# Kernel optimization log

Hardware: AMD Instinct MI355X
Metric: run time of the kernel (lower is better)

Reference implementation:

```python
import jax, jax.numpy as jnp
import numpy as np

D = 1024
KERNEL = 4

def setup_inputs() -> dict:
    key = jax.random.key(0)
    ks = jax.random.split(key, 8)
    B, L, d = 4, 8192, D
    x = jax.random.normal(ks[0], (B, L, d), dtype=jnp.float32)
    conv_weight = jax.random.normal(ks[1], (d, 1, KERNEL), dtype=jnp.float32) * 0.02
    conv_bias = jnp.zeros((d,), dtype=jnp.float32)
    lim = 1.0 / np.sqrt(d)
    Wr_w = jax.random.uniform(ks[2], (d, d), jnp.float32, -lim, lim)
    Wr_b = jax.random.uniform(ks[3], (d,), jnp.float32, -lim, lim)
    Wi_w = jax.random.uniform(ks[4], (d, d), jnp.float32, -lim, lim)
    Wi_b = jax.random.uniform(ks[5], (d,), jnp.float32, -lim, lim)
    log_a = jnp.full((d,), 7.5, dtype=jnp.float32)
    out_w = jax.random.uniform(ks[6], (d, d), jnp.float32, -lim, lim)
    norm_w = jnp.ones((d,), dtype=jnp.float32)
    return {"x": x, "conv_weight": conv_weight, "conv_bias": conv_bias,
            "Wr_w": Wr_w, "Wr_b": Wr_b, "Wi_w": Wi_w, "Wi_b": Wi_b,
            "log_a": log_a, "out_w": out_w, "norm_w": norm_w}

def _causal_depthwise_conv(x, w, b):
    # x: [B,L,d], w: [d,1,K], b: [d]. out[t] = sum_k w[:,0,k] * x[t-3+k] + b
    B, L, d = x.shape
    xp = jnp.pad(x, ((0, 0), (KERNEL - 1, 0), (0, 0)))
    out = b[None, None, :]
    for k in range(KERNEL):  # small fixed kernel loop
        out = out + xp[:, k:k + L, :] * w[:, 0, k][None, None, :]
    return out

def _parallel_scan(a_t, b_t):
    # h_t = a_t * h_{t-1} + b_t via log-space cumsum; float32 throughout
    a = a_t.astype(jnp.float32)
    b = b_t.astype(jnp.float32)
    log_A = jnp.clip(jnp.cumsum(jnp.log(jnp.clip(a, 1e-7)), axis=1), -80.0, None)
    A = jnp.exp(log_A)
    h = A * jnp.cumsum(b * jnp.exp(-log_A), axis=1)
    return h.astype(a_t.dtype)

def _rmsnorm(x, w, eps=1e-6):
    ms = jnp.mean(jnp.square(x.astype(jnp.float32)), axis=-1, keepdims=True)
    return (x * jax.lax.rsqrt(ms + eps)).astype(x.dtype) * w

def reference(x, conv_weight, conv_bias, Wr_w, Wr_b, Wi_w, Wi_b, log_a, out_w, norm_w):
    x_conv = _causal_depthwise_conv(x, conv_weight, conv_bias)          # [B,L,d]
    r_t = jax.nn.sigmoid(x_conv @ Wr_w.T + Wr_b)
    i_t = jax.nn.sigmoid(x_conv @ Wi_w.T + Wi_b)
    a_base = jax.nn.sigmoid(log_a.astype(jnp.float32)).astype(x.dtype)
    a_t = jnp.power(a_base[None, None, :], 8.0 * r_t)
    b_t = jnp.sqrt(jnp.clip(1.0 - a_t * a_t, 1e-6, None)) * (i_t * x_conv)
    h = _parallel_scan(a_t, b_t)
    return _rmsnorm(h @ out_w.T, norm_w)
```

## Files before the change

### kernel.cpp

```cpp
#include <hip/hip_runtime.h>
#include <hip/hip_bf16.h>

#define D 1024
#define KW 4
#define SEQL 8192
#define BATCH 4
#define MROWS (BATCH*SEQL)
#define SEG 32
#define NSEG (SEQL/SEG)
#define NCHAIN (BATCH*D)

using bf16 = __hip_bfloat16;
typedef __attribute__((ext_vector_type(8))) short bf16x8_t;
typedef __attribute__((ext_vector_type(4))) float f32x4_t;

__device__ __forceinline__ float sigmoid_f(float x){ return 1.0f/(1.0f + __expf(-x)); }

__device__ __forceinline__ void gload_lds16(const bf16* g, bf16* l){
  __builtin_amdgcn_global_load_lds(
    (const __attribute__((address_space(1))) unsigned int*)g,
    (__attribute__((address_space(3))) unsigned int*)l,
    16, 0, 0);
}

__device__ __forceinline__ void bf16x2_unpack(unsigned int u, float& lo, float& hi){
  union { unsigned int i; float f; } a, b;
  a.i = (u & 0xffffu) << 16;
  b.i = u & 0xffff0000u;
  lo = a.f; hi = b.f;
}
__device__ __forceinline__ unsigned int bf16x2_pack(float lo, float hi){
  unsigned short l = __builtin_bit_cast(unsigned short, __float2bfloat16(lo));
  unsigned short h = __builtin_bit_cast(unsigned short, __float2bfloat16(hi));
  return (unsigned int)l | ((unsigned int)h << 16);
}

__global__ __launch_bounds__(256) void prep_k(const float* __restrict__ Wr, const float* __restrict__ Wi,
                                              const float* __restrict__ Wrb, const float* __restrict__ Wib,
                                              const float* __restrict__ Wo,
                                              bf16* __restrict__ W1, bf16* __restrict__ Wob,
                                              float* __restrict__ b1){
  int idx = blockIdx.x*256 + threadIdx.x;
  if (idx < 2*D*D){
    int n = idx >> 10;
    float v = (n < D) ? Wr[idx] : Wi[idx - D*D];
    W1[idx] = __float2bfloat16(v);
  } else if (idx < 3*D*D){
    int j = idx - 2*D*D;
    Wob[j] = __float2bfloat16(Wo[j]);
  }
  if (idx < 2*D){
    b1[idx] = (idx < D) ? Wrb[idx] : Wib[idx - D];
  }
}

__global__ __launch_bounds__(256) void conv_k(const float* __restrict__ x, const float* __restrict__ w,
                                              const float* __restrict__ bias,
                                              unsigned int* __restrict__ xcb){
  int idx = blockIdx.x*256 + threadIdx.x;
  int c4 = idx & 255;
  int c  = c4 * 4;
  int mm = idx >> 8;
  int m  = mm * 2;
  int l  = m & (SEQL-1);
  const float* wp = w + c*KW;
  f32x4_t t0 = *(const f32x4_t*)(wp);
  f32x4_t t1 = *(const f32x4_t*)(wp + 4);
  f32x4_t t2 = *(const f32x4_t*)(wp + 8);
  f32x4_t t3 = *(const f32x4_t*)(wp + 12);
  f32x4_t bb = *(const f32x4_t*)(bias + c);
  const float* xm = x + (size_t)m*D + c;
  f32x4_t z  = (f32x4_t){0.f,0.f,0.f,0.f};
  f32x4_t r4 = *(const f32x4_t*)(xm + D);
  f32x4_t r3 = *(const f32x4_t*)(xm);
  f32x4_t r2 = (l>=1)? *(const f32x4_t*)(xm - D)   : z;
  f32x4_t r1 = (l>=2)? *(const f32x4_t*)(xm - 2*D) : z;
  f32x4_t r0 = (l>=3)? *(const f32x4_t*)(xm - 3*D) : z;
  float a0 = bb[0] + t0[0]*r0[0] + t0[1]*r1[0] + t0[2]*r2[0] + t0[3]*r3[0];
  float a1 = bb[1] + t1[0]*r0[1] + t1[1]*r1[1] + t1[2]*r2[1] + t1[3]*r3[1];
  float a2 = bb[2] + t2[0]*r0[2] + t2[1]*r1[2] + t2[2]*r2[2] + t2[3]*r3[2];
  float a3 = bb[3] + t3[0]*r0[3] + t3[1]*r1[3] + t3[2]*r2[3] + t3[3]*r3[3];
  float b0 = bb[0] + t0[0]*r1[0] + t0[1]*r2[0] + t0[2]*r3[0] + t0[3]*r4[0];
  float b1v= bb[1] + t1[0]*r1[1] + t1[1]*r2[1] + t1[2]*r3[1] + t1[3]*r4[1];
  float b2 = bb[2] + t2[0]*r1[2] + t2[1]*r2[2] + t2[2]*r3[2] + t2[3]*r4[2];
  float b3 = bb[3] + t3[0]*r1[3] + t3[1]*r2[3] + t3[2]*r3[3] + t3[3]*r4[3];
  uint2 o0, o1;
  o0.x = bf16x2_pack(a0, a1); o0.y = bf16x2_pack(a2, a3);
  o1.x = bf16x2_pack(b0, b1v); o1.y = bf16x2_pack(b2, b3);
  *(uint2*)(xcb + (size_t)m*512 + 2*c4)       = o0;
  *(uint2*)(xcb + (size_t)(m+1)*512 + 2*c4)   = o1;
}

template<typename OutT> __device__ __forceinline__ void store_cvt(OutT* p, float v);
template<> __device__ __forceinline__ void store_cvt<float>(float* p, float v){ *p = v; }
template<> __device__ __forceinline__ void store_cvt<bf16>(bf16* p, float v){ *p = __float2bfloat16(v); }

#define MFMA_BF16(a,b,c) __builtin_amdgcn_mfma_f32_16x16x32_bf16((a),(b),(c),0,0,0)

#define GPHASE(buf, q, STAGE_STMT, WAIT_STMT) do{                         \
    bf16x8_t a0 = rdA(buf, 2*(q),   0);                                   \
    bf16x8_t a1 = rdA(buf, 2*(q),   1);                                   \
    bf16x8_t a2 = rdA(buf, 2*(q)+1, 0);                                   \
    bf16x8_t a3 = rdA(buf, 2*(q)+1, 1);                                   \
    if ((q) == 0){                                                        \
      b00 = rdB(buf,0,0); b01 = rdB(buf,0,1);                             \
      b10 = rdB(buf,1,0); b11 = rdB(buf,1,1);                             \
      b20 = rdB(buf,2,0); b21 = rdB(buf,2,1);                             \
      b30 = rdB(buf,3,0); b31 = rdB(buf,3,1);                             \
    }                                                                     \
    STAGE_STMT;                                                           \
    WAIT_STMT;                                                            \
    __builtin_amdgcn_s_barrier();                                         \
    asm volatile("s_waitcnt lgkmcnt(0)" ::: "memory");                    \
    __builtin_amdgcn_s_setprio(1);                                        \
    acc[2*(q)  ][0] = MFMA_BF16(a0, b00, acc[2*(q)  ][0]);                \
    acc[2*(q)  ][1] = MFMA_BF16(a0, b10, acc[2*(q)  ][1]);                \
    acc[2*(q)  ][2] = MFMA_BF16(a0, b20, acc[2*(q)  ][2]);                \
    acc[2*(q)  ][3] = MFMA_BF16(a0, b30, acc[2*(q)  ][3]);                \
    acc[2*(q)+1][0] = MFMA_BF16(a2, b00, acc[2*(q)+1][0]);                \
    acc[2*(q)+1][1] = MFMA_BF16(a2, b10, acc[2*(q)+1][1]);                \
    acc[2*(q)+1][2] = MFMA_BF16(a2, b20, acc[2*(q)+1][2]);                \
    acc[2*(q)+1][3] = MFMA_BF16(a2, b30, acc[2*(q)+1][3]);                \
    acc[2*(q)  ][0] = MFMA_BF16(a1, b01, acc[2*(q)  ][0]);                \
    acc[2*(q)  ][1] = MFMA_BF16(a1, b11, acc[2*(q)  ][1]);                \
    acc[2*(q)  ][2] = MFMA_BF16(a1, b21, acc[2*(q)  ][2]);                \
    acc[2*(q)  ][3] = MFMA_BF16(a1, b31, acc[2*(q)  ][3]);                \
    acc[2*(q)+1][0] = MFMA_BF16(a3, b01, acc[2*(q)+1][0]);                \
    acc[2*(q)+1][1] = MFMA_BF16(a3, b11, acc[2*(q)+1][1]);                \
    acc[2*(q)+1][2] = MFMA_BF16(a3, b21, acc[2*(q)+1][2]);                \
    acc[2*(q)+1][3] = MFMA_BF16(a3, b31, acc[2*(q)+1][3]);                \
    __builtin_amdgcn_s_setprio(0);                                        \
    __builtin_amdgcn_s_barrier();                                         \
}while(0)

#define WAIT_STEADY do{ if (it + 1 < nIter) asm volatile("s_waitcnt vmcnt(4)" ::: "memory"); \
                        else                asm volatile("s_waitcnt vmcnt(0)" ::: "memory"); }while(0)

template<typename OutT, bool HB>
__global__ __launch_bounds__(512, 2) void gemm256(const bf16* __restrict__ A, const bf16* __restrict__ B,
                                                  const float* __restrict__ bias, OutT* __restrict__ C,
                                                  int M, int N, int K){
  __shared__ alignas(128) bf16 Asm[2][256*64];
  __shared__ alignas(128) bf16 Bsm[2][256*64];
  const int t    = threadIdx.x;
  const int wave = t >> 6, lane = t & 63;
  const int wm   = wave >> 2, wn = wave & 3;
  const int lrow = lane & 15, quad = lane >> 4;

  const int nbn = N >> 8;
  const int cpx = gridDim.x >> 3;
  const int bid = blockIdx.x;
  const int swz = (bid & 7) * cpx + (bid >> 3);
  const int m0  = (swz / nbn) << 8;
  const int n0  = (swz % nbn) << 8;

  const int srow = wave*8 + (lane >> 3);
  const int scol = (((lane & 7) ^ (srow & 7)) << 3);

  auto stageA = [&](int tile, int half, int buf){
    const bf16* g = A + (size_t)(m0 + half*128 + srow)*K + tile*64 + scol;
    bf16* l = &Asm[buf][half*128*64 + wave*8*64];
    gload_lds16(g, l);
    gload_lds16(g + (size_t)64*K, l + 64*64);
  };
  auto stageB = [&](int tile, int half, int buf){
    const bf16* g = B + (size_t)(n0 + half*128 + srow)*K + tile*64 + scol;
    bf16* l = &Bsm[buf][half*128*64 + wave*8*64];
    gload_lds16(g, l);
    gload_lds16(g + (size_t)64*K, l + 64*64);
  };
  auto rdA = [&](int buf, int fi, int ks)->bf16x8_t{
    return *(const bf16x8_t*)&Asm[buf][(wm*128 + fi*16 + lrow)*64 + ((((ks)*4 + quad) ^ (lrow & 7)) << 3)];
  };
  auto rdB = [&](int buf, int j, int ks)->bf16x8_t{
    return *(const bf16x8_t*)&Bsm[buf][(wn*64 + j*16 + lrow)*64 + ((((ks)*4 + quad) ^ (lrow & 7)) << 3)];
  };

  f32x4_t acc[8][4];
  #pragma unroll
  for (int i=0;i<8;i++)
    #pragma unroll
    for (int j=0;j<4;j++) acc[i][j] = (f32x4_t){0.f,0.f,0.f,0.f};
  bf16x8_t b00,b01,b10,b11,b20,b21,b30,b31;

  const int nt    = K >> 6;
  const int nIter = nt >> 1;

  stageB(0, 0, 0); stageB(0, 1, 0);
  stageA(0, 0, 0); stageA(0, 1, 0);
  stageB(1, 0, 1); stageB(1, 1, 1);
  asm volatile("s_waitcnt vmcnt(4)" ::: "memory");
  __builtin_amdgcn_s_barrier();

  for (int it = 0; it < nIter; ++it){
    const int t1 = 2*it + 1, t2 = 2*it + 2, t3 = 2*it + 3;
    const bool ok2 = (t2 < nt), ok3 = (t3 < nt);
    GPHASE(0, 0, stageA(t1, 0, 1), );
    GPHASE(0, 1, stageA(t1, 1, 1), );
    GPHASE(0, 2, if (ok2) stageB(t2, 0, 0), );
    GPHASE(0, 3, if (ok2) stageB(t2, 1, 0), WAIT_STEADY);
    GPHASE(1, 0, if (ok2) stageA(t2, 0, 0), );
    GPHASE(1, 1, if (ok2) stageA(t2, 1, 0), );
    GPHASE(1, 2, if (ok3) stageB(t3, 0, 1), );
    GPHASE(1, 3, if (ok3) stageB(t3, 1, 1), WAIT_STEADY);
  }

  constexpr int ROWP = 256 + 16/(int)sizeof(OutT);
  OutT* tile = (OutT*)&Asm[0][0];
  const int trow = t >> 4;
  const int tcol = (t & 15) * 16;
  float bvj[4];
  #pragma unroll
  for (int j=0;j<4;j++) bvj[j] = HB ? bias[n0 + wn*64 + j*16 + lrow] : 0.f;
  const int grow = m0 + (trow >> 4)*128 + (trow & 15);

  #pragma unroll
  for (int i=0;i<8;i++){
    __builtin_amdgcn_s_barrier();
    #pragma unroll
    for (int j=0;j<4;j++){
      int lcol = wn*64 + j*16 + lrow;
      #pragma unroll
      for (int r=0;r<4;r++)
        store_cvt(&tile[(wm*16 + quad*4 + r)*ROWP + lcol], acc[i][j][r] + bvj[j]);
    }
    __builtin_amdgcn_s_barrier();
    const int4* lp = (const int4*)&tile[trow*ROWP + tcol];
    int4* gp = (int4*)&C[(size_t)(grow + i*16)*N + n0 + tcol];
    #pragma unroll
    for (int q=0; q<(int)sizeof(OutT); ++q) gp[q] = lp[q];
  }
}

__global__ __launch_bounds__(256) void scan1_k(const unsigned int* __restrict__ ri,
                                               const unsigned int* __restrict__ xcb,
                                               const float* __restrict__ log_a,
                                               float* __restrict__ AprodT, float* __restrict__ HendT){
  int idx = blockIdx.x*256 + threadIdx.x;
  int c4 = idx & 255;
  int c  = c4*4;
  int bs = idx >> 8;
  int s  = bs & (NSEG-1);
  int b  = bs >> 8;
  size_t m0 = (size_t)b*SEQL + (size_t)s*SEG;
  f32x4_t la = *(const f32x4_t*)(log_a + c);
  float c1[4];
  #pragma unroll
  for (int j=0;j<4;j++) c1[j] = -8.f * log1pf(__expf(-la[j]));
  float A[4] = {1.f,1.f,1.f,1.f};
  float h[4] = {0.f,0.f,0.f,0.f};
  #pragma unroll 4
  for (int l=0; l<SEG; l++){
    size_t m = m0 + l;
    uint2 uzr = *(const uint2*)(ri  + m*1024 + 2*c4);
    uint2 uzi = *(const uint2*)(ri  + m*1024 + 512 + 2*c4);
    uint2 uxv = *(const uint2*)(xcb + m*512  + 2*c4);
    float zr[4], zi[4], xv[4];
    bf16x2_unpack(uzr.x, zr[0], zr[1]); bf16x2_unpack(uzr.y, zr[2], zr[3]);
    bf16x2_unpack(uzi.x, zi[0], zi[1]); bf16x2_unpack(uzi.y, zi[2], zi[3]);
    bf16x2_unpack(uxv.x, xv[0], xv[1]); bf16x2_unpack(uxv.y, xv[2], xv[3]);
    #pragma unroll
    for (int j=0;j<4;j++){
      float a  = __expf(c1[j] * sigmoid_f(zr[j]));
      float bt = sqrtf(fmaxf(1.f - a*a, 1e-6f)) * sigmoid_f(zi[j]) * xv[j];
      A[j] *= a;
      h[j]  = fmaf(a, h[j], bt);
    }
  }
  size_t tbase = (size_t)s*NCHAIN + (size_t)b*D + c;
  *(f32x4_t*)(AprodT + tbase) = (f32x4_t){A[0],A[1],A[2],A[3]};
  *(f32x4_t*)(HendT  + tbase) = (f32x4_t){h[0],h[1],h[2],h[3]};
}

__global__ __launch_bounds__(256) void scan2_k(const float* __restrict__ AprodT, const float* __restrict__ HendT,
                                               float* __restrict__ carryT){
  int gid   = blockIdx.x*256 + threadIdx.x;
  int chain = gid >> 6;
  int lane  = gid & 63;
  int s0    = lane*4;
  float a[4], e[4];
  #pragma unroll
  for (int k=0;k<4;k++){
    a[k] = AprodT[(size_t)(s0+k)*NCHAIN + chain];
    e[k] = HendT [(size_t)(s0+k)*NCHAIN + chain];
  }
  float A = a[0], H = e[0];
  #pragma unroll
  for (int k=1;k<4;k++){ H = fmaf(a[k], H, e[k]); A *= a[k]; }
  #pragma unroll
  for (int off=1; off<64; off<<=1){
    float Ao = __shfl_up(A, off, 64);
    float Ho = __shfl_up(H, off, 64);
    if (lane >= off){ H = fmaf(A, Ho, H); A = A*Ao; }
  }
  float Hx = __shfl_up(H, 1, 64);
  if (lane == 0) Hx = 0.f;
  float h = Hx;
  #pragma unroll
  for (int k=0;k<4;k++){
    carryT[(size_t)(s0+k)*NCHAIN + chain] = h;
    h = fmaf(a[k], h, e[k]);
  }
}

__global__ __launch_bounds__(256) void scan3_k(const unsigned int* __restrict__ ri,
                                               unsigned int* xcb,
                                               const float* __restrict__ log_a, const float* __restrict__ carryT){
  int idx = blockIdx.x*256 + threadIdx.x;
  int c4 = idx & 255;
  int c  = c4*4;
  int bs = idx >> 8;
  int s  = bs & (NSEG-1);
  int b  = bs >> 8;
  size_t m0 = (size_t)b*SEQL + (size_t)s*SEG;
  f32x4_t la = *(const f32x4_t*)(log_a + c);
  float c1[4];
  #pragma unroll
  for (int j=0;j<4;j++) c1[j] = -8.f * log1pf(__expf(-la[j]));
  f32x4_t h4 = *(const f32x4_t*)(carryT + (size_t)s*NCHAIN + (size_t)b*D + c);
  float h[4] = {h4[0], h4[1], h4[2], h4[3]};
  #pragma unroll 4
  for (int l=0; l<SEG; l++){
    size_t m = m0 + l;
    uint2 uzr = *(const uint2*)(ri  + m*1024 + 2*c4);
    uint2 uzi = *(const uint2*)(ri  + m*1024 + 512 + 2*c4);
    uint2 uxv = *(const uint2*)(xcb + m*512  + 2*c4);
    float zr[4], zi[4], xv[4];
    bf16x2_unpack(uzr.x, zr[0], zr[1]); bf16x2_unpack(uzr.y, zr[2], zr[3]);
    bf16x2_unpack(uzi.x, zi[0], zi[1]); bf16x2_unpack(uzi.y, zi[2], zi[3]);
    bf16x2_unpack(uxv.x, xv[0], xv[1]); bf16x2_unpack(uxv.y, xv[2], xv[3]);
    #pragma unroll
    for (int j=0;j<4;j++){
      float a  = __expf(c1[j] * sigmoid_f(zr[j]));
      float bt = sqrtf(fmaxf(1.f - a*a, 1e-6f)) * sigmoid_f(zi[j]) * xv[j];
      h[j] = fmaf(a, h[j], bt);
    }
    uint2 o;
    o.x = bf16x2_pack(h[0], h[1]);
    o.y = bf16x2_pack(h[2], h[3]);
    *(uint2*)(xcb + m*512 + 2*c4) = o;
  }
}

__global__ __launch_bounds__(256) void rms_k(float* __restrict__ y, const float* __restrict__ nw){
  int wave = threadIdx.x >> 6, lane = threadIdx.x & 63;
  size_t row = (size_t)blockIdx.x*4 + wave;
  float* yr = y + row*D;
  f32x4_t v[4];
  #pragma unroll
  for (int q=0;q<4;q++) v[q] = *(const f32x4_t*)(yr + q*256 + lane*4);
  float ss = 0.f;
  #pragma unroll
  for (int q=0;q<4;q++) ss += v[q][0]*v[q][0] + v[q][1]*v[q][1] + v[q][2]*v[q][2] + v[q][3]*v[q][3];
  #pragma unroll
  for (int off=32; off>0; off>>=1) ss += __shfl_xor(ss, off, 64);
  float scale = rsqrtf(ss * (1.f/D) + 1e-6f);
  #pragma unroll
  for (int q=0;q<4;q++){
    f32x4_t w = *(const f32x4_t*)(nw + q*256 + lane*4);
    f32x4_t o;
    #pragma unroll
    for (int k=0;k<4;k++) o[k] = v[q][k]*scale*w[k];
    *(f32x4_t*)(yr + q*256 + lane*4) = o;
  }
}

extern "C" void kernel_launch(void* const* d_in, const int* in_sizes, int n_in,
                              void* d_out, int out_size, void* d_ws, size_t ws_size,
                              hipStream_t stream) {
  const float* x     = (const float*)d_in[0];
  const float* convw = (const float*)d_in[1];
  const float* convb = (const float*)d_in[2];
  const float* Wr_w  = (const float*)d_in[3];
  const float* Wr_b  = (const float*)d_in[4];
  const float* Wi_w  = (const float*)d_in[5];
  const float* Wi_b  = (const float*)d_in[6];
  const float* log_a = (const float*)d_in[7];
  const float* out_w = (const float*)d_in[8];
  const float* norm_w= (const float*)d_in[9];

  char* ws = (char*)d_ws;
  size_t off = 0;
  auto alloc = [&](size_t bytes)->char*{ char* p = ws + off; off += (bytes + 255) & ~(size_t)255; return p; };

  bf16*  xcb   = (bf16*) alloc((size_t)MROWS*D*2);
  bf16*  ri    = (bf16*) alloc((size_t)MROWS*2*D*2);
  bf16*  W1    = (bf16*) alloc((size_t)2*D*D*2);
  bf16*  Wob   = (bf16*) alloc((size_t)D*D*2);
  float* b1    = (float*)alloc((size_t)2*D*4);
  float* AprodT= (float*)alloc((size_t)NSEG*NCHAIN*4);
  float* HendT = (float*)alloc((size_t)NSEG*NCHAIN*4);
  float* carryT= (float*)alloc((size_t)NSEG*NCHAIN*4);
  float* y     = (float*)d_out;

  prep_k<<<dim3((3*D*D + 255)/256), dim3(256), 0, stream>>>(Wr_w, Wi_w, Wr_b, Wi_b, out_w, W1, Wob, b1);
  conv_k<<<dim3((MROWS/2)*(D/4)/256), dim3(256), 0, stream>>>(x, convw, convb, (unsigned int*)xcb);
  gemm256<bf16, true><<<dim3((MROWS/256)*((2*D)/256)), dim3(512), 0, stream>>>(xcb, W1, b1, ri, MROWS, 2*D, D);
  scan1_k<<<dim3(BATCH*NSEG*(D/4)/256), dim3(256), 0, stream>>>((const unsigned int*)ri, (const unsigned int*)xcb, log_a, AprodT, HendT);
  scan2_k<<<dim3(NCHAIN*64/256), dim3(256), 0, stream>>>(AprodT, HendT, carryT);
  scan3_k<<<dim3(BATCH*NSEG*(D/4)/256), dim3(256), 0, stream>>>((const unsigned int*)ri, (unsigned int*)xcb, log_a, carryT);
  gemm256<float, false><<<dim3((MROWS/256)*(D/256)), dim3(512), 0, stream>>>(xcb, Wob, nullptr, y, MROWS, D, D);
  rms_k<<<dim3(MROWS/4), dim3(256), 0, stream>>>(y, norm_w);
}
```

Measured before the change: 674.6 us.

## Fuse gate activations into GEMM epilogue with interleaved Wr/Wi output

Interleaves Wr and Wi rows in the packed weight so each GEMM output pair holds (zr, zi) for one channel. The GEMM epilogue then computes the decay a and input term b_t, reading xconv itself, and writes packed bf16 (1-a, b_t). This removes the repeated sigmoid/exp/sqrt work and the extra xconv reads from both scan passes, and the scans now read one 16-byte load per step. The cost is a heavier GEMM epilogue and storing 1-a in bf16, which may change rounding of a near 1.

Result: faster. 657.8 us (-2.5%).

```diff
diff --git a/kernel.cpp b/kernel.cpp
--- a/kernel.cpp
+++ b/kernel.cpp
@@ -37,20 +37,26 @@
 
 __global__ __launch_bounds__(256) void prep_k(const float* __restrict__ Wr, const float* __restrict__ Wi,
                                               const float* __restrict__ Wrb, const float* __restrict__ Wib,
-                                              const float* __restrict__ Wo,
+                                              const float* __restrict__ Wo, const float* __restrict__ log_a,
                                               bf16* __restrict__ W1, bf16* __restrict__ Wob,
-                                              float* __restrict__ b1){
+                                              float* __restrict__ b1, float* __restrict__ c1buf){
   int idx = blockIdx.x*256 + threadIdx.x;
   if (idx < 2*D*D){
-    int n = idx >> 10;
-    float v = (n < D) ? Wr[idx] : Wi[idx - D*D];
+    int n   = idx >> 10;
+    int col = idx & 1023;
+    int c   = n >> 1;
+    float v = (n & 1) ? Wi[(size_t)c*D + col] : Wr[(size_t)c*D + col];
     W1[idx] = __float2bfloat16(v);
   } else if (idx < 3*D*D){
     int j = idx - 2*D*D;
     Wob[j] = __float2bfloat16(Wo[j]);
   }
   if (idx < 2*D){
-    b1[idx] = (idx < D) ? Wrb[idx] : Wib[idx - D];
+    int c = idx >> 1;
+    b1[idx] = (idx & 1) ? Wib[c] : Wrb[c];
+  }
+  if (idx < D){
+    c1buf[idx] = -8.f * log1pf(__expf(-log_a[idx]));
   }
 }
 
@@ -136,10 +142,12 @@
 #define WAIT_STEADY do{ if (it + 1 < nIter) asm volatile("s_waitcnt vmcnt(4)" ::: "memory"); \
                         else                asm volatile("s_waitcnt vmcnt(0)" ::: "memory"); }while(0)
 
-template<typename OutT, bool HB>
+template<typename OutT, bool HB, bool FUSE>
 __global__ __launch_bounds__(512, 2) void gemm256(const bf16* __restrict__ A, const bf16* __restrict__ B,
                                                   const float* __restrict__ bias, OutT* __restrict__ C,
-                                                  int M, int N, int K){
+                                                  int M, int N, int K,
+                                                  const bf16* __restrict__ xv_src,
+                                                  const float* __restrict__ c1buf){
   __shared__ alignas(128) bf16 Asm[2][256*64];
   __shared__ alignas(128) bf16 Bsm[2][256*64];
   const int t    = threadIdx.x;
@@ -214,6 +222,16 @@
   for (int j=0;j<4;j++) bvj[j] = HB ? bias[n0 + wn*64 + j*16 + lrow] : 0.f;
   const int grow = m0 + (trow >> 4)*128 + (trow & 15);
 
+  int cbase = 0;
+  float c1v[8];
+  if constexpr (FUSE){
+    cbase = (n0 + tcol) >> 1;
+    f32x4_t c1a = *(const f32x4_t*)(c1buf + cbase);
+    f32x4_t c1b = *(const f32x4_t*)(c1buf + cbase + 4);
+    #pragma unroll
+    for (int k=0;k<4;k++){ c1v[k] = c1a[k]; c1v[4+k] = c1b[k]; }
+  }
+
   #pragma unroll
   for (int i=0;i<8;i++){
     __builtin_amdgcn_s_barrier();
@@ -226,15 +244,36 @@
     }
     __builtin_amdgcn_s_barrier();
     const int4* lp = (const int4*)&tile[trow*ROWP + tcol];
-    int4* gp = (int4*)&C[(size_t)(grow + i*16)*N + n0 + tcol];
-    #pragma unroll
-    for (int q=0; q<(int)sizeof(OutT); ++q) gp[q] = lp[q];
-  }
-}
-
-__global__ __launch_bounds__(256) void scan1_k(const unsigned int* __restrict__ ri,
-                                               const unsigned int* __restrict__ xcb,
-                                               const float* __restrict__ log_a,
+    if constexpr (FUSE){
+      int4 w0 = lp[0], w1 = lp[1];
+      unsigned int lw[8] = {(unsigned)w0.x,(unsigned)w0.y,(unsigned)w0.z,(unsigned)w0.w,
+                            (unsigned)w1.x,(unsigned)w1.y,(unsigned)w1.z,(unsigned)w1.w};
+      const int row = grow + i*16;
+      uint4 xv4 = *(const uint4*)(xv_src + (size_t)row*D + cbase);
+      float xv[8];
+      bf16x2_unpack(xv4.x, xv[0], xv[1]); bf16x2_unpack(xv4.y, xv[2], xv[3]);
+      bf16x2_unpack(xv4.z, xv[4], xv[5]); bf16x2_unpack(xv4.w, xv[6], xv[7]);
+      unsigned int out[8];
+      #pragma unroll
+      for (int k=0;k<8;k++){
+        float zr, zi;
+        bf16x2_unpack(lw[k], zr, zi);
+        float a  = __expf(c1v[k] * sigmoid_f(zr));
+        float bt = sqrtf(fmaxf(1.f - a*a, 1e-6f)) * sigmoid_f(zi) * xv[k];
+        out[k] = bf16x2_pack(1.f - a, bt);
+      }
+      int4* gp = (int4*)&C[(size_t)row*N + n0 + tcol];
+      gp[0] = make_int4(out[0],out[1],out[2],out[3]);
+      gp[1] = make_int4(out[4],out[5],out[6],out[7]);
+    } else {
+      int4* gp = (int4*)&C[(size_t)(grow + i*16)*N + n0 + tcol];
+      #pragma unroll
+      for (int q=0; q<(int)sizeof(OutT); ++q) gp[q] = lp[q];
+    }
+  }
+}
+
+__global__ __launch_bounds__(256) void scan1_k(const unsigned int* __restrict__ ab,
                                                float* __restrict__ AprodT, float* __restrict__ HendT){
   int idx = blockIdx.x*256 + threadIdx.x;
   int c4 = idx & 255;
@@ -243,26 +282,17 @@
   int s  = bs & (NSEG-1);
   int b  = bs >> 8;
   size_t m0 = (size_t)b*SEQL + (size_t)s*SEG;
-  f32x4_t la = *(const f32x4_t*)(log_a + c);
-  float c1[4];
-  #pragma unroll
-  for (int j=0;j<4;j++) c1[j] = -8.f * log1pf(__expf(-la[j]));
   float A[4] = {1.f,1.f,1.f,1.f};
   float h[4] = {0.f,0.f,0.f,0.f};
   #pragma unroll 4
   for (int l=0; l<SEG; l++){
-    size_t m = m0 + l;
-    uint2 uzr = *(const uint2*)(ri  + m*1024 + 2*c4);
-    uint2 uzi = *(const uint2*)(ri  + m*1024 + 512 + 2*c4);
-    uint2 uxv = *(const uint2*)(xcb + m*512  + 2*c4);
-    float zr[4], zi[4], xv[4];
-    bf16x2_unpack(uzr.x, zr[0], zr[1]); bf16x2_unpack(uzr.y, zr[2], zr[3]);
-    bf16x2_unpack(uzi.x, zi[0], zi[1]); bf16x2_unpack(uzi.y, zi[2], zi[3]);
-    bf16x2_unpack(uxv.x, xv[0], xv[1]); bf16x2_unpack(uxv.y, xv[2], xv[3]);
+    uint4 u = *(const uint4*)(ab + (m0 + l)*1024 + 4*c4);
+    unsigned int uu[4] = {u.x, u.y, u.z, u.w};
     #pragma unroll
     for (int j=0;j<4;j++){
-      float a  = __expf(c1[j] * sigmoid_f(zr[j]));
-      float bt = sqrtf(fmaxf(1.f - a*a, 1e-6f)) * sigmoid_f(zi[j]) * xv[j];
+      float dv, bt;
+      bf16x2_unpack(uu[j], dv, bt);
+      float a = 1.f - dv;
       A[j] *= a;
       h[j]  = fmaf(a, h[j], bt);
     }
@@ -303,9 +333,9 @@
   }
 }
 
-__global__ __launch_bounds__(256) void scan3_k(const unsigned int* __restrict__ ri,
-                                               unsigned int* xcb,
-                                               const float* __restrict__ log_a, const float* __restrict__ carryT){
+__global__ __launch_bounds__(256) void scan3_k(const unsigned int* __restrict__ ab,
+                                               unsigned int* __restrict__ hout,
+                                               const float* __restrict__ carryT){
   int idx = blockIdx.x*256 + threadIdx.x;
   int c4 = idx & 255;
   int c  = c4*4;
@@ -313,32 +343,23 @@
   int s  = bs & (NSEG-1);
   int b  = bs >> 8;
   size_t m0 = (size_t)b*SEQL + (size_t)s*SEG;
-  f32x4_t la = *(const f32x4_t*)(log_a + c);
-  float c1[4];
-  #pragma unroll
-  for (int j=0;j<4;j++) c1[j] = -8.f * log1pf(__expf(-la[j]));
   f32x4_t h4 = *(const f32x4_t*)(carryT + (size_t)s*NCHAIN + (size_t)b*D + c);
   float h[4] = {h4[0], h4[1], h4[2], h4[3]};
   #pragma unroll 4
   for (int l=0; l<SEG; l++){
     size_t m = m0 + l;
-    uint2 uzr = *(const uint2*)(ri  + m*1024 + 2*c4);
-    uint2 uzi = *(const uint2*)(ri  + m*1024 + 512 + 2*c4);
-    uint2 uxv = *(const uint2*)(xcb + m*512  + 2*c4);
-    float zr[4], zi[4], xv[4];
-    bf16x2_unpack(uzr.x, zr[0], zr[1]); bf16x2_unpack(uzr.y, zr[2], zr[3]);
-    bf16x2_unpack(uzi.x, zi[0], zi[1]); bf16x2_unpack(uzi.y, zi[2], zi[3]);
-    bf16x2_unpack(uxv.x, xv[0], xv[1]); bf16x2_unpack(uxv.y, xv[2], xv[3]);
+    uint4 u = *(const uint4*)(ab + m*1024 + 4*c4);
+    unsigned int uu[4] = {u.x, u.y, u.z, u.w};
     #pragma unroll
     for (int j=0;j<4;j++){
-      float a  = __expf(c1[j] * sigmoid_f(zr[j]));
-      float bt = sqrtf(fmaxf(1.f - a*a, 1e-6f)) * sigmoid_f(zi[j]) * xv[j];
-      h[j] = fmaf(a, h[j], bt);
+      float dv, bt;
+      bf16x2_unpack(uu[j], dv, bt);
+      h[j] = fmaf(1.f - dv, h[j], bt);
     }
     uint2 o;
     o.x = bf16x2_pack(h[0], h[1]);
     o.y = bf16x2_pack(h[2], h[3]);
-    *(uint2*)(xcb + m*512 + 2*c4) = o;
+    *(uint2*)(hout + m*512 + 2*c4) = o;
   }
 }
 
@@ -384,21 +405,22 @@
   auto alloc = [&](size_t bytes)->char*{ char* p = ws + off; off += (bytes + 255) & ~(size_t)255; return p; };
 
   bf16*  xcb   = (bf16*) alloc((size_t)MROWS*D*2);
-  bf16*  ri    = (bf16*) alloc((size_t)MROWS*2*D*2);
+  bf16*  ab    = (bf16*) alloc((size_t)MROWS*2*D*2);
   bf16*  W1    = (bf16*) alloc((size_t)2*D*D*2);
   bf16*  Wob   = (bf16*) alloc((size_t)D*D*2);
   float* b1    = (float*)alloc((size_t)2*D*4);
+  float* c1buf = (float*)alloc((size_t)D*4);
   float* AprodT= (float*)alloc((size_t)NSEG*NCHAIN*4);
   float* HendT = (float*)alloc((size_t)NSEG*NCHAIN*4);
   float* carryT= (float*)alloc((size_t)NSEG*NCHAIN*4);
   float* y     = (float*)d_out;
 
-  prep_k<<<dim3((3*D*D + 255)/256), dim3(256), 0, stream>>>(Wr_w, Wi_w, Wr_b, Wi_b, out_w, W1, Wob, b1);
+  prep_k<<<dim3((3*D*D + 255)/256), dim3(256), 0, stream>>>(Wr_w, Wi_w, Wr_b, Wi_b, out_w, log_a, W1, Wob, b1, c1buf);
   conv_k<<<dim3((MROWS/2)*(D/4)/256), dim3(256), 0, stream>>>(x, convw, convb, (unsigned int*)xcb);
-  gemm256<bf16, true><<<dim3((MROWS/256)*((2*D)/256)), dim3(512), 0, stream>>>(xcb, W1, b1, ri, MROWS, 2*D, D);
-  scan1_k<<<dim3(BATCH*NSEG*(D/4)/256), dim3(256), 0, stream>>>((const unsigned int*)ri, (const unsigned int*)xcb, log_a, AprodT, HendT);
+  gemm256<bf16, true, true><<<dim3((MROWS/256)*((2*D)/256)), dim3(512), 0, stream>>>(xcb, W1, b1, ab, MROWS, 2*D, D, xcb, c1buf);
+  scan1_k<<<dim3(BATCH*NSEG*(D/4)/256), dim3(256), 0, stream>>>((const unsigned int*)ab, AprodT, HendT);
   scan2_k<<<dim3(NCHAIN*64/256), dim3(256), 0, stream>>>(AprodT, HendT, carryT);
-  scan3_k<<<dim3(BATCH*NSEG*(D/4)/256), dim3(256), 0, stream>>>((const unsigned int*)ri, (unsigned int*)xcb, log_a, carryT);
-  gemm256<float, false><<<dim3((MROWS/256)*(D/256)), dim3(512), 0, stream>>>(xcb, Wob, nullptr, y, MROWS, D, D);
+  scan3_k<<<dim3(BATCH*NSEG*(D/4)/256), dim3(256), 0, stream>>>((const unsigned int*)ab, (unsigned int*)xcb, carryT);
+  gemm256<float, false, false><<<dim3((MROWS/256)*(D/256)), dim3(512), 0, stream>>>(xcb, Wob, nullptr, y, MROWS, D, D, nullptr, nullptr);
   rms_k<<<dim3(MROWS/4), dim3(256), 0, stream>>>(y, norm_w);
 }
```
